# Optimization experiments

Hardware: AMD Instinct MI355X
Metric: run time of the kernel (lower is better)

Reference implementation:

```python
import jax, jax.numpy as jnp
import numpy as np

DIST_THD = 2.0  # squared-distance threshold from my_chamfer_fn


def setup_inputs() -> dict:
    key = jax.random.key(0)
    k1, k2 = jax.random.split(key)
    pc1 = jax.random.normal(k1, (1, 16384, 3), dtype=jnp.float32)
    pc2 = jax.random.normal(k2, (1, 16384, 3), dtype=jnp.float32)
    return {"pc1": pc1, "pc2": pc2}


def _chamfer(x, y):
    # x: (N, P1, D), y: (N, P2, D). Squared pairwise distances (as pytorch3d knn_points).
    x2 = jnp.sum(x * x, axis=-1)                       # (N, P1)
    y2 = jnp.sum(y * y, axis=-1)                       # (N, P2)
    xy = jnp.einsum('npd,nqd->npq', x, y)              # (N, P1, P2)
    d2 = x2[:, :, None] + y2[:, None, :] - 2.0 * xy    # (N, P1, P2)
    cham_x = jnp.min(d2, axis=2)                       # (N, P1) NN dist x->y (K=1)
    cham_y = jnp.min(d2, axis=1)                       # (N, P2) NN dist y->x
    # threshold mask: distances >= 2 are zeroed
    cham_x = jnp.where(cham_x >= DIST_THD, 0.0, cham_x)
    cham_y = jnp.where(cham_y >= DIST_THD, 0.0, cham_y)
    N, P1, _ = x.shape
    P2 = y.shape[1]
    # point_reduction='mean' (lengths are full P), batch_reduction='mean'
    cx = jnp.sum(cham_x, axis=1) / P1
    cy = jnp.sum(cham_y, axis=1) / P2
    return jnp.sum(cx) / N + jnp.sum(cy) / N


def reference(pc1, pc2):
    # Chamfer loss between pc1 and pc2 (the kernel inside NSFP optimization);
    # normals are unused in this code path, so only the distance loss is returned.
    return _chamfer(pc1, pc2)
```

## Files before the change

kernel.cpp:

```cpp
#include <hip/hip_runtime.h>
#include <hip/hip_bf16.h>


constexpr int P      = 16384;
constexpr int BLK    = 256;
constexpr int NSEG   = 16;
constexpr int SEGPTS = P / NSEG;
constexpr int ROUND  = 1024;
constexpr int TILES  = ROUND / 32;
constexpr int ROWSB  = 256;
constexpr int CLOUDB = P * 32;

typedef short s8v  __attribute__((ext_vector_type(8)));
typedef float f16v __attribute__((ext_vector_type(16)));

static __device__ inline unsigned short bf16r(float f) {
    unsigned u = __float_as_uint(f);
    u = (u + 0x7FFFu + ((u >> 16) & 1u)) >> 16;
    return (unsigned short)u;
}
static __device__ inline float bf2f(unsigned short h) {
    return __uint_as_float(((unsigned)h) << 16);
}

static __device__ inline void encA(float a, float b, float c, unsigned e[8]) {
    const unsigned ONE = 0x3F80u;
    const float s = fmaf(a, a, fmaf(b, b, c * c));
    const unsigned short ah = bf16r(a), bh = bf16r(b), ch = bf16r(c);
    const unsigned short al = bf16r(a - bf2f(ah));
    const unsigned short bl = bf16r(b - bf2f(bh));
    const unsigned short cl = bf16r(c - bf2f(ch));
    const unsigned short sh = bf16r(s), sl = bf16r(s - bf2f(sh));
    e[0] = ah | ((unsigned)al << 16);
    e[1] = bh | ((unsigned)bl << 16);
    e[2] = ch | ((unsigned)cl << 16);
    e[3] = ah | ((unsigned)bh << 16);
    e[4] = ch | ((unsigned)sh << 16);
    e[5] = sl | (ONE << 16);
    e[6] = ONE;
    e[7] = 0;
}

static __device__ inline void encB(float a, float b, float c, unsigned e[8]) {
    const unsigned ONE = 0x3F80u;
    const float s = fmaf(a, a, fmaf(b, b, c * c));
    const unsigned short ah = bf16r(a), bh = bf16r(b), ch = bf16r(c);
    const unsigned short al = bf16r(a - bf2f(ah));
    const unsigned short bl = bf16r(b - bf2f(bh));
    const unsigned short cl = bf16r(c - bf2f(ch));
    const unsigned short sh = bf16r(s), sl = bf16r(s - bf2f(sh));
    const unsigned short Ah = bf16r(-2.f * bf2f(ah)), Bh = bf16r(-2.f * bf2f(bh));
    const unsigned short Ch = bf16r(-2.f * bf2f(ch));
    const unsigned short Al = bf16r(-2.f * bf2f(al)), Bl = bf16r(-2.f * bf2f(bl));
    const unsigned short Cl = bf16r(-2.f * bf2f(cl));
    e[0] = Ah | ((unsigned)Ah << 16);
    e[1] = Bh | ((unsigned)Bh << 16);
    e[2] = Ch | ((unsigned)Ch << 16);
    e[3] = Al | ((unsigned)Bl << 16);
    e[4] = Cl | (ONE << 16);
    e[5] = ONE | ((unsigned)sh << 16);
    e[6] = sl;
    e[7] = 0;
}

__global__ __launch_bounds__(BLK) void encode_pts(
    const float* __restrict__ pc1, const float* __restrict__ pc2,
    unsigned char* __restrict__ encAbuf, unsigned char* __restrict__ encBbuf,
    float* __restrict__ out)
{
    const int gid = blockIdx.x * BLK + threadIdx.x;
    if (gid == 0) out[0] = 0.0f;
    const int c = gid >> 14;
    const int p = gid & (P - 1);
    const float* src = c ? pc2 : pc1;
    const float x = src[3 * p], y = src[3 * p + 1], z = src[3 * p + 2];

    unsigned ea[8], eb[8];
    encA(x, y, z, ea);
    encB(x, y, z, eb);

    unsigned char* ap = encAbuf + (size_t)c * CLOUDB + (size_t)p * 32;
    *(uint4*)(ap)      = make_uint4(ea[0], ea[1], ea[2], ea[3]);
    *(uint4*)(ap + 16) = make_uint4(ea[4], ea[5], ea[6], ea[7]);

    unsigned char* bp = encBbuf + (size_t)c * CLOUDB + (size_t)(p >> 5) * 1024
                        + (size_t)(p & 31) * 16;
    *(uint4*)(bp)       = make_uint4(eb[0], eb[1], eb[2], eb[3]);
    *(uint4*)(bp + 512) = make_uint4(eb[4], eb[5], eb[6], eb[7]);
}

__global__ __launch_bounds__(BLK, 4) void chamfer_mfma(
    const unsigned char* __restrict__ encAbuf,
    const unsigned char* __restrict__ encBbuf,
    float* __restrict__ part)
{
    const int dir = blockIdx.z;
    const int acloud = dir;
    const int bcloud = dir ^ 1;

    __shared__ __align__(16) unsigned char ytile[ROUND * 32];

    const int tid  = threadIdx.x;
    const int lane = tid & 63;
    const int wv   = tid >> 6;
    const int l31  = lane & 31;
    const int half = lane >> 5;

    const int rowbase = blockIdx.x * ROWSB + wv * 64;
    const unsigned char* abase = encAbuf + (size_t)acloud * CLOUDB + (size_t)half * 16;
    s8v afrag0 = *(const s8v*)(abase + (size_t)(rowbase + l31) * 32);
    s8v afrag1 = *(const s8v*)(abase + (size_t)(rowbase + 32 + l31) * 32);

    {
        const uint4* gs = (const uint4*)(encBbuf + (size_t)bcloud * CLOUDB
                                         + (size_t)(blockIdx.y * SEGPTS) * 32);
        uint4* ls = (uint4*)ytile;
        #pragma unroll
        for (int j = 0; j < 8; ++j) {
            const int idx = tid + j * BLK;
            ls[idx] = gs[idx];
        }
    }

    f16v acc0, acc1, Z;
    #pragma unroll
    for (int i = 0; i < 16; ++i) { acc0[i] = 3.0e38f; acc1[i] = 3.0e38f; Z[i] = 0.0f; }

    __syncthreads();

    const unsigned char* rp = ytile + lane * 16;
    for (int t = 0; t < TILES; t += 2) {
        const s8v b0 = *(const s8v*)(rp + t * 1024);
        const s8v b1 = *(const s8v*)(rp + t * 1024 + 1024);
        {
            const f16v da = __builtin_amdgcn_mfma_f32_32x32x16_bf16(afrag0, b0, Z, 0, 0, 0);
            const f16v db = __builtin_amdgcn_mfma_f32_32x32x16_bf16(afrag0, b1, Z, 0, 0, 0);
            #pragma unroll
            for (int i = 0; i < 16; ++i)
                acc0[i] = fminf(acc0[i], fminf(da[i], db[i]));
        }
        {
            const f16v da = __builtin_amdgcn_mfma_f32_32x32x16_bf16(afrag1, b0, Z, 0, 0, 0);
            const f16v db = __builtin_amdgcn_mfma_f32_32x32x16_bf16(afrag1, b1, Z, 0, 0, 0);
            #pragma unroll
            for (int i = 0; i < 16; ++i)
                acc1[i] = fminf(acc1[i], fminf(da[i], db[i]));
        }
    }

    float* pbase = part + ((size_t)(dir * NSEG + blockIdx.y)) * P;
    #pragma unroll
    for (int s = 0; s < 2; ++s) {
        #pragma unroll
        for (int rg = 0; rg < 16; ++rg) {
            float v = s ? acc1[rg] : acc0[rg];
            v = fminf(v, __shfl_xor(v, 1, 64));
            v = fminf(v, __shfl_xor(v, 2, 64));
            v = fminf(v, __shfl_xor(v, 4, 64));
            v = fminf(v, __shfl_xor(v, 8, 64));
            v = fminf(v, __shfl_xor(v, 16, 64));
            if (l31 == 0) {
                const int row = rowbase + s * 32 + (rg & 3) + 8 * (rg >> 2) + 4 * half;
                pbase[row] = v;
            }
        }
    }
}

__global__ __launch_bounds__(BLK) void chamfer_reduce(
    const float* __restrict__ part, float* __restrict__ out)
{
    const int gid = blockIdx.x * BLK + threadIdx.x;
    const int dirbase = (gid >= P) ? NSEG * P : 0;
    const int row = gid & (P - 1);

    float m = part[dirbase + row];
    #pragma unroll
    for (int s = 1; s < NSEG; ++s) m = fminf(m, part[dirbase + s * P + row]);

    if (m >= 2.0f) m = 0.0f;
    float v = m * (1.0f / (float)P);

    #pragma unroll
    for (int off = 32; off > 0; off >>= 1) v += __shfl_down(v, off, 64);

    __shared__ float wsum[BLK / 64];
    const int lane = threadIdx.x & 63;
    const int wvi = threadIdx.x >> 6;
    if (lane == 0) wsum[wvi] = v;
    __syncthreads();
    if (threadIdx.x == 0) {
        float ssum = wsum[0];
        #pragma unroll
        for (int w = 1; w < BLK / 64; ++w) ssum += wsum[w];
        atomicAdd(out, ssum);
    }
}

extern "C" void kernel_launch(void* const* d_in, const int* in_sizes, int n_in,
                              void* d_out, int out_size, void* d_ws, size_t ws_size,
                              hipStream_t stream) {
    const float* pc1 = (const float*)d_in[0];
    const float* pc2 = (const float*)d_in[1];
    float* out = (float*)d_out;
    unsigned char* ws = (unsigned char*)d_ws;
    float* part = (float*)ws;
    unsigned char* encBbuf = ws + (2u << 20);
    unsigned char* encAbuf = ws + (3u << 20);

    encode_pts<<<(2 * P) / BLK, BLK, 0, stream>>>(pc1, pc2, encAbuf, encBbuf, out);

    dim3 grid(P / ROWSB, NSEG, 2);
    chamfer_mfma<<<grid, BLK, 0, stream>>>(encAbuf, encBbuf, part);
    chamfer_reduce<<<(2 * P) / BLK, BLK, 0, stream>>>(part, out);
}
```

Measured before the change: 88.12 us.

## Compute distance matrix once and derive both row and column minima

Instead of launching both chamfer directions and recomputing the pairwise distance tiles twice, the kernel computes pc1-vs-pc2 tiles once and reduces both the per-row minima and per-column minima from the same MFMA outputs. Column minima are written per wave into a large partial buffer and reduced across all row slices in the final reduction kernel. This halves matrix work but adds extra in-loop reductions, shuffles, global stores and a much larger partial buffer to read back.

```diff
diff --git a/kernel.cpp b/kernel.cpp
--- a/kernel.cpp
+++ b/kernel.cpp
@@ -4,11 +4,12 @@
 
 constexpr int P      = 16384;
 constexpr int BLK    = 256;
-constexpr int NSEG   = 16;
-constexpr int SEGPTS = P / NSEG;
-constexpr int ROUND  = 1024;
-constexpr int TILES  = ROUND / 32;
+constexpr int NSEGC  = 16;
+constexpr int SEGPTS = P / NSEGC;
+constexpr int TILES  = SEGPTS / 32;
 constexpr int ROWSB  = 256;
+constexpr int NROWB  = P / ROWSB;
+constexpr int NSLICE = NROWB * 4;
 constexpr int CLOUDB = P * 32;
 
 typedef short s8v  __attribute__((ext_vector_type(8)));
@@ -21,6 +22,16 @@
 }
 static __device__ inline float bf2f(unsigned short h) {
     return __uint_as_float(((unsigned)h) << 16);
+}
+static __device__ inline float tree16(const f16v d) {
+    float a0 = fminf(d[0], d[1]),  a1 = fminf(d[2], d[3]);
+    float a2 = fminf(d[4], d[5]),  a3 = fminf(d[6], d[7]);
+    float a4 = fminf(d[8], d[9]),  a5 = fminf(d[10], d[11]);
+    float a6 = fminf(d[12], d[13]), a7 = fminf(d[14], d[15]);
+    a0 = fminf(a0, a1); a2 = fminf(a2, a3);
+    a4 = fminf(a4, a5); a6 = fminf(a6, a7);
+    a0 = fminf(a0, a2); a4 = fminf(a4, a6);
+    return fminf(a0, a4);
 }
 
 static __device__ inline void encA(float a, float b, float c, unsigned e[8]) {
@@ -65,40 +76,37 @@
 
 __global__ __launch_bounds__(BLK) void encode_pts(
     const float* __restrict__ pc1, const float* __restrict__ pc2,
-    unsigned char* __restrict__ encAbuf, unsigned char* __restrict__ encBbuf,
+    unsigned char* __restrict__ encA1, unsigned char* __restrict__ encB2,
     float* __restrict__ out)
 {
     const int gid = blockIdx.x * BLK + threadIdx.x;
     if (gid == 0) out[0] = 0.0f;
-    const int c = gid >> 14;
     const int p = gid & (P - 1);
-    const float* src = c ? pc2 : pc1;
-    const float x = src[3 * p], y = src[3 * p + 1], z = src[3 * p + 2];
-
-    unsigned ea[8], eb[8];
-    encA(x, y, z, ea);
-    encB(x, y, z, eb);
-
-    unsigned char* ap = encAbuf + (size_t)c * CLOUDB + (size_t)p * 32;
-    *(uint4*)(ap)      = make_uint4(ea[0], ea[1], ea[2], ea[3]);
-    *(uint4*)(ap + 16) = make_uint4(ea[4], ea[5], ea[6], ea[7]);
-
-    unsigned char* bp = encBbuf + (size_t)c * CLOUDB + (size_t)(p >> 5) * 1024
-                        + (size_t)(p & 31) * 16;
-    *(uint4*)(bp)       = make_uint4(eb[0], eb[1], eb[2], eb[3]);
-    *(uint4*)(bp + 512) = make_uint4(eb[4], eb[5], eb[6], eb[7]);
+    if (gid < P) {
+        unsigned ea[8];
+        encA(pc1[3 * p], pc1[3 * p + 1], pc1[3 * p + 2], ea);
+        unsigned char* ap = encA1 + (size_t)p * 32;
+        *(uint4*)(ap)      = make_uint4(ea[0], ea[1], ea[2], ea[3]);
+        *(uint4*)(ap + 16) = make_uint4(ea[4], ea[5], ea[6], ea[7]);
+    } else {
+        unsigned eb[8];
+        encB(pc2[3 * p], pc2[3 * p + 1], pc2[3 * p + 2], eb);
+        unsigned char* bp = encB2 + (size_t)(p >> 5) * 1024 + (size_t)(p & 31) * 16;
+        *(uint4*)(bp)       = make_uint4(eb[0], eb[1], eb[2], eb[3]);
+        *(uint4*)(bp + 512) = make_uint4(eb[4], eb[5], eb[6], eb[7]);
+    }
 }
 
 __global__ __launch_bounds__(BLK, 4) void chamfer_mfma(
-    const unsigned char* __restrict__ encAbuf,
-    const unsigned char* __restrict__ encBbuf,
-    float* __restrict__ part)
+    const unsigned char* __restrict__ encA1,
+    const unsigned char* __restrict__ encB2,
+    float* __restrict__ part_x,
+    float* __restrict__ part_y)
 {
-    const int dir = blockIdx.z;
-    const int acloud = dir;
-    const int bcloud = dir ^ 1;
-
-    __shared__ __align__(16) unsigned char ytile[ROUND * 32];
+    const int bx = blockIdx.x;
+    const int by = blockIdx.y;
+
+    __shared__ __align__(16) unsigned char ytile[SEGPTS * 32];
 
     const int tid  = threadIdx.x;
     const int lane = tid & 63;
@@ -106,14 +114,13 @@
     const int l31  = lane & 31;
     const int half = lane >> 5;
 
-    const int rowbase = blockIdx.x * ROWSB + wv * 64;
-    const unsigned char* abase = encAbuf + (size_t)acloud * CLOUDB + (size_t)half * 16;
-    s8v afrag0 = *(const s8v*)(abase + (size_t)(rowbase + l31) * 32);
-    s8v afrag1 = *(const s8v*)(abase + (size_t)(rowbase + 32 + l31) * 32);
+    const int rowbase = bx * ROWSB + wv * 64;
+    const unsigned char* abase = encA1 + (size_t)half * 16;
+    const s8v afrag0 = *(const s8v*)(abase + (size_t)(rowbase + l31) * 32);
+    const s8v afrag1 = *(const s8v*)(abase + (size_t)(rowbase + 32 + l31) * 32);
 
     {
-        const uint4* gs = (const uint4*)(encBbuf + (size_t)bcloud * CLOUDB
-                                         + (size_t)(blockIdx.y * SEGPTS) * 32);
+        const uint4* gs = (const uint4*)(encB2 + (size_t)(by * SEGPTS) * 32);
         uint4* ls = (uint4*)ytile;
         #pragma unroll
         for (int j = 0; j < 8; ++j) {
@@ -128,27 +135,34 @@
 
     __syncthreads();
 
+    float* ybase = part_y + (size_t)((bx << 2) + wv) * P + by * SEGPTS;
     const unsigned char* rp = ytile + lane * 16;
     for (int t = 0; t < TILES; t += 2) {
         const s8v b0 = *(const s8v*)(rp + t * 1024);
         const s8v b1 = *(const s8v*)(rp + t * 1024 + 1024);
+        const f16v d0a = __builtin_amdgcn_mfma_f32_32x32x16_bf16(afrag0, b0, Z, 0, 0, 0);
+        const f16v d0b = __builtin_amdgcn_mfma_f32_32x32x16_bf16(afrag0, b1, Z, 0, 0, 0);
+        const f16v d1a = __builtin_amdgcn_mfma_f32_32x32x16_bf16(afrag1, b0, Z, 0, 0, 0);
+        const f16v d1b = __builtin_amdgcn_mfma_f32_32x32x16_bf16(afrag1, b1, Z, 0, 0, 0);
+        #pragma unroll
+        for (int i = 0; i < 16; ++i)
+            acc0[i] = fminf(acc0[i], fminf(d0a[i], d0b[i]));
+        #pragma unroll
+        for (int i = 0; i < 16; ++i)
+            acc1[i] = fminf(acc1[i], fminf(d1a[i], d1b[i]));
         {
-            const f16v da = __builtin_amdgcn_mfma_f32_32x32x16_bf16(afrag0, b0, Z, 0, 0, 0);
-            const f16v db = __builtin_amdgcn_mfma_f32_32x32x16_bf16(afrag0, b1, Z, 0, 0, 0);
-            #pragma unroll
-            for (int i = 0; i < 16; ++i)
-                acc0[i] = fminf(acc0[i], fminf(da[i], db[i]));
+            float c = fminf(tree16(d0a), tree16(d1a));
+            c = fminf(c, __shfl_xor(c, 32, 64));
+            if (lane < 32) ybase[t * 32 + l31] = c;
         }
         {
-            const f16v da = __builtin_amdgcn_mfma_f32_32x32x16_bf16(afrag1, b0, Z, 0, 0, 0);
-            const f16v db = __builtin_amdgcn_mfma_f32_32x32x16_bf16(afrag1, b1, Z, 0, 0, 0);
-            #pragma unroll
-            for (int i = 0; i < 16; ++i)
-                acc1[i] = fminf(acc1[i], fminf(da[i], db[i]));
-        }
-    }
-
-    float* pbase = part + ((size_t)(dir * NSEG + blockIdx.y)) * P;
+            float c = fminf(tree16(d0b), tree16(d1b));
+            c = fminf(c, __shfl_xor(c, 32, 64));
+            if (lane < 32) ybase[(t + 1) * 32 + l31] = c;
+        }
+    }
+
+    float* pbase = part_x + (size_t)by * P;
     #pragma unroll
     for (int s = 0; s < 2; ++s) {
         #pragma unroll
@@ -168,15 +182,21 @@
 }
 
 __global__ __launch_bounds__(BLK) void chamfer_reduce(
-    const float* __restrict__ part, float* __restrict__ out)
+    const float* __restrict__ part_x, const float* __restrict__ part_y,
+    float* __restrict__ out)
 {
     const int gid = blockIdx.x * BLK + threadIdx.x;
-    const int dirbase = (gid >= P) ? NSEG * P : 0;
-    const int row = gid & (P - 1);
-
-    float m = part[dirbase + row];
-    #pragma unroll
-    for (int s = 1; s < NSEG; ++s) m = fminf(m, part[dirbase + s * P + row]);
+    float m;
+    if (gid < P) {
+        m = part_x[gid];
+        #pragma unroll
+        for (int s = 1; s < NSEGC; ++s) m = fminf(m, part_x[(size_t)s * P + gid]);
+    } else {
+        const int j = gid - P;
+        m = part_y[j];
+        #pragma unroll 8
+        for (int s = 1; s < NSLICE; ++s) m = fminf(m, part_y[(size_t)s * P + j]);
+    }
 
     if (m >= 2.0f) m = 0.0f;
     float v = m * (1.0f / (float)P);
@@ -204,13 +224,14 @@
     const float* pc2 = (const float*)d_in[1];
     float* out = (float*)d_out;
     unsigned char* ws = (unsigned char*)d_ws;
-    float* part = (float*)ws;
-    unsigned char* encBbuf = ws + (2u << 20);
-    unsigned char* encAbuf = ws + (3u << 20);
-
-    encode_pts<<<(2 * P) / BLK, BLK, 0, stream>>>(pc1, pc2, encAbuf, encBbuf, out);
-
-    dim3 grid(P / ROWSB, NSEG, 2);
-    chamfer_mfma<<<grid, BLK, 0, stream>>>(encAbuf, encBbuf, part);
-    chamfer_reduce<<<(2 * P) / BLK, BLK, 0, stream>>>(part, out);
-}
+    float* part_x = (float*)ws;
+    float* part_y = (float*)(ws + (1u << 20));
+    unsigned char* encA1 = ws + (17u << 20);
+    unsigned char* encB2 = ws + (17u << 20) + (512u << 10);
+
+    encode_pts<<<(2 * P) / BLK, BLK, 0, stream>>>(pc1, pc2, encA1, encB2, out);
+
+    dim3 grid(NROWB, NSEGC);
+    chamfer_mfma<<<grid, BLK, 0, stream>>>(encA1, encB2, part_x, part_y);
+    chamfer_reduce<<<(2 * P) / BLK, BLK, 0, stream>>>(part_x, part_y, out);
+}
```

After: 131.4 us. +49.1%, slower.
